# Kernel tuning notes

Hardware: AMD Instinct MI355X
Metric: run time of the kernel (lower is better)

## Reference

```python
import jax, jax.numpy as jnp
import numpy as np

TEMPERATURE = 1.0  # module default current_temperature
TOP_K = 2
NUM_EXPERTS = 64
EPS = 1e-10


def setup_inputs() -> dict:
    key = jax.random.key(0)
    k1, k2 = jax.random.split(key)
    x = jax.random.normal(k1, (4, 4096, 2048), dtype=jnp.float32)
    # nn.Linear(d_model, num_experts) weight has shape [num_experts, d_model]
    W_gate = jax.random.normal(k2, (NUM_EXPERTS, 2048), dtype=jnp.float32) * (1.0 / np.sqrt(2048))
    return {"x": x, "W_gate": W_gate}


def reference(x, W_gate):
    # Gate GEMM: [B,S,D] x [E,D] -> [B,S,E]
    logits = jnp.einsum("bsd,ed->bse", x, W_gate)
    scaled = logits / TEMPERATURE
    # Full distribution over experts (for load-balancing loss)
    router_probs = jax.nn.softmax(scaled, axis=-1)
    # Top-k selection over the expert dim, then renormalize via softmax
    top_k_logits, top_k_indices = jax.lax.top_k(scaled, TOP_K)  # [B,S,K]
    top_k_weights = jax.nn.softmax(top_k_logits, axis=-1)
    # Routing stats (no-grad in torch; plain values here)
    entropy = -jnp.sum(router_probs * jnp.log(router_probs + EPS), axis=-1)
    routing_entropy = entropy.mean()
    selection_confidence = top_k_weights[:, :, 0].mean()
    counts = jnp.zeros((NUM_EXPERTS,), dtype=x.dtype).at[top_k_indices.reshape(-1)].add(1.0)
    expert_utilization = counts / (counts.sum() + EPS)
    return (top_k_weights, top_k_indices, router_probs,
            routing_entropy, selection_confidence, expert_utilization)
```

## Files before the change

kernel.cpp:

```cpp
#include <hip/hip_runtime.h>
#include <math.h>

#define NTOK 16384
#define DIM 2048
#define NEXP 64
#define TB 32
#define NSG 32

#define OFF_W    0
#define OFF_I    32768
#define OFF_P    65536
#define OFF_ENT  1114112
#define OFF_CONF 1114113
#define OFF_UTIL 1114114

typedef short s16x8 __attribute__((ext_vector_type(8)));
typedef float f32x4 __attribute__((ext_vector_type(4)));

__device__ __forceinline__ unsigned short f2bf(float v) {
    unsigned u = __builtin_bit_cast(unsigned, v);
    u = u + 0x7FFFu + ((u >> 16) & 1u);
    return (unsigned short)(u >> 16);
}
__device__ __forceinline__ float bf2f(unsigned short b) {
    return __builtin_bit_cast(float, (unsigned)b << 16);
}

__global__ void router_wsplit(const float* __restrict__ Wg, uint4* __restrict__ wsp,
                              float* __restrict__ out) {
    const int c = blockIdx.x;
    const int t = threadIdx.x;
    if (c == 0 && t < 66) out[OFF_ENT + t] = 0.0f;
    const int nt = t >> 6, l = t & 63;
    const int e  = 16 * nt + (l & 15);
    const int k0 = 32 * c + 8 * (l >> 4);
    const float* src = Wg + (size_t)e * DIM + k0;
    float4 a = *(const float4*)src;
    float4 b = *(const float4*)(src + 4);
    float v[8] = {a.x, a.y, a.z, a.w, b.x, b.y, b.z, b.w};
    unsigned short H[8], M[8], L[8];
    #pragma unroll
    for (int j = 0; j < 8; ++j) {
        H[j] = f2bf(v[j]);  float r = v[j] - bf2f(H[j]);
        M[j] = f2bf(r);     r = r - bf2f(M[j]);
        L[j] = f2bf(r);
    }
    uint4 ph, pm, pl;
    ph.x = H[0] | ((unsigned)H[1] << 16); ph.y = H[2] | ((unsigned)H[3] << 16);
    ph.z = H[4] | ((unsigned)H[5] << 16); ph.w = H[6] | ((unsigned)H[7] << 16);
    pm.x = M[0] | ((unsigned)M[1] << 16); pm.y = M[2] | ((unsigned)M[3] << 16);
    pm.z = M[4] | ((unsigned)M[5] << 16); pm.w = M[6] | ((unsigned)M[7] << 16);
    pl.x = L[0] | ((unsigned)L[1] << 16); pl.y = L[2] | ((unsigned)L[3] << 16);
    pl.z = L[4] | ((unsigned)L[5] << 16); pl.w = L[6] | ((unsigned)L[7] << 16);
    const int idx = c * 256 + t;
    wsp[idx]         = ph;
    wsp[16384 + idx] = pm;
    wsp[32768 + idx] = pl;
}

#define LOADW(W_, c_) { const int b_ = (c_)*256 + np*128 + l;  \
    W_[0] = wq[b_];          W_[1] = wq[b_ + 64];              \
    W_[2] = wq[16384 + b_];  W_[3] = wq[16384 + b_ + 64];      \
    W_[4] = wq[32768 + b_];  W_[5] = wq[32768 + b_ + 64]; }

#define SPLIT8(a0_, a1_, ph_, pm_, pl_) {                                \
    float xv[8] = {a0_.x, a0_.y, a0_.z, a0_.w,                           \
                   a1_.x, a1_.y, a1_.z, a1_.w};                          \
    unsigned hw_[8], mw_[8], lw_[8];                                     \
    _Pragma("unroll")                                                    \
    for (int j = 0; j < 8; ++j) {                                        \
        unsigned u_  = __builtin_bit_cast(unsigned, xv[j]);              \
        unsigned hb_ = u_ & 0xFFFF0000u;                                 \
        float    r_  = xv[j] - __builtin_bit_cast(float, hb_);           \
        unsigned mb_ = __builtin_bit_cast(unsigned, r_) & 0xFFFF0000u;   \
        float    r2_ = r_ - __builtin_bit_cast(float, mb_);              \
        unsigned lb_ = __builtin_bit_cast(unsigned, r2_);                \
        hw_[j] = hb_ >> 16; mw_[j] = mb_ >> 16; lw_[j] = lb_ >> 16;      \
    }                                                                    \
    ph_.x = hw_[0] | (hw_[1] << 16); ph_.y = hw_[2] | (hw_[3] << 16);    \
    ph_.z = hw_[4] | (hw_[5] << 16); ph_.w = hw_[6] | (hw_[7] << 16);    \
    pm_.x = mw_[0] | (mw_[1] << 16); pm_.y = mw_[2] | (mw_[3] << 16);    \
    pm_.z = mw_[4] | (mw_[5] << 16); pm_.w = mw_[6] | (mw_[7] << 16);    \
    pl_.x = lw_[0] | (lw_[1] << 16); pl_.y = lw_[2] | (lw_[3] << 16);    \
    pl_.z = lw_[4] | (lw_[5] << 16); pl_.w = lw_[6] | (lw_[7] << 16);    \
}

#define STAGEW(buf_) {                                                   \
    uint4 ph_, pm_, pl_;                                                 \
    SPLIT8(xr0, xr1, ph_, pm_, pl_);                                     \
    Xp[g][buf_][0][cc][st][sq] = ph_;                                    \
    Xp[g][buf_][1][cc][st][sq] = pm_;                                    \
    Xp[g][buf_][2][cc][st][sq] = pl_;                                    \
}

#define READA(buf_, cc_) {                                               \
    ah = __builtin_bit_cast(s16x8, Xp[g][buf_][0][cc_][tl][sl]);         \
    am = __builtin_bit_cast(s16x8, Xp[g][buf_][1][cc_][tl][sl]);         \
    al = __builtin_bit_cast(s16x8, Xp[g][buf_][2][cc_][tl][sl]);         \
}

#define COMPUTE(W_) {                                                    \
    s16x8 b0h_ = __builtin_bit_cast(s16x8, W_[0]);                       \
    s16x8 b1h_ = __builtin_bit_cast(s16x8, W_[1]);                       \
    s16x8 b0m_ = __builtin_bit_cast(s16x8, W_[2]);                       \
    s16x8 b1m_ = __builtin_bit_cast(s16x8, W_[3]);                       \
    s16x8 b0l_ = __builtin_bit_cast(s16x8, W_[4]);                       \
    s16x8 b1l_ = __builtin_bit_cast(s16x8, W_[5]);                       \
    acc0 = __builtin_amdgcn_mfma_f32_16x16x32_bf16(ah, b0h_, acc0, 0, 0, 0); \
    acc1 = __builtin_amdgcn_mfma_f32_16x16x32_bf16(ah, b1h_, acc1, 0, 0, 0); \
    acc0 = __builtin_amdgcn_mfma_f32_16x16x32_bf16(am, b0h_, acc0, 0, 0, 0); \
    acc1 = __builtin_amdgcn_mfma_f32_16x16x32_bf16(am, b1h_, acc1, 0, 0, 0); \
    acc0 = __builtin_amdgcn_mfma_f32_16x16x32_bf16(ah, b0m_, acc0, 0, 0, 0); \
    acc1 = __builtin_amdgcn_mfma_f32_16x16x32_bf16(ah, b1m_, acc1, 0, 0, 0); \
    acc0 = __builtin_amdgcn_mfma_f32_16x16x32_bf16(am, b0m_, acc0, 0, 0, 0); \
    acc1 = __builtin_amdgcn_mfma_f32_16x16x32_bf16(am, b1m_, acc1, 0, 0, 0); \
    acc0 = __builtin_amdgcn_mfma_f32_16x16x32_bf16(ah, b0l_, acc0, 0, 0, 0); \
    acc1 = __builtin_amdgcn_mfma_f32_16x16x32_bf16(ah, b1l_, acc1, 0, 0, 0); \
    acc0 = __builtin_amdgcn_mfma_f32_16x16x32_bf16(al, b0h_, acc0, 0, 0, 0); \
    acc1 = __builtin_amdgcn_mfma_f32_16x16x32_bf16(al, b1h_, acc1, 0, 0, 0); \
    }

__global__ __launch_bounds__(512, 4) void router_main(
    const float* __restrict__ x, const uint4* __restrict__ wq,
    float* __restrict__ out)
{
    __shared__ __align__(16) uint4 Xp[2][2][3][2][TB][4];
    __shared__ float lg[TB][NEXP + 1];
    __shared__ float m1s[TB], rss[TB];
    __shared__ float s_ent, s_conf, s_cnt[NEXP];

    const int tid = threadIdx.x;
    const int l   = tid & 63;
    const int w   = tid >> 6;
    const int g   = tid >> 8;
    const int lw  = w & 3;
    const int np  = __builtin_amdgcn_readfirstlane(lw >> 1);
    const int tt  = lw & 1;
    const int qd  = l >> 4;
    const int tl  = tt * 16 + (l & 15);
    const int sl  = qd ^ ((tl >> 2) & 3);
    const int t0  = blockIdx.x * TB;
    const int cb  = g * NSG;

    if (tid == 0) { s_ent = 0.0f; s_conf = 0.0f; }
    if (tid < NEXP) s_cnt[tid] = 0.0f;

    const int gtid = tid & 255;
    const int cc  = gtid >> 7;
    const int rr  = gtid & 127;
    const int st  = rr >> 2;
    const int sq  = rr & 3;
    const int gq  = sq ^ ((st >> 2) & 3);
    const float* xsrc = x + (size_t)(t0 + st) * DIM + 32 * cb + 8 * gq;

    f32x4 acc0 = (f32x4)(0.0f), acc1 = (f32x4)(0.0f);
    s16x8 ah, am, al;
    uint4 wA[6], wB[6];
    float4 xr0, xr1;

    xr0 = *(const float4*)(xsrc + cc * 32);
    xr1 = *(const float4*)(xsrc + cc * 32 + 4);
    LOADW(wA, cb + 0); LOADW(wB, cb + 1);
    STAGEW(0);
    xr0 = *(const float4*)(xsrc + (2 + cc) * 32);
    xr1 = *(const float4*)(xsrc + (2 + cc) * 32 + 4);
    __syncthreads();

    for (int s = 0; s < NSG; s += 2) {
        const int buf = (s >> 1) & 1;
        if (s + 2 < NSG) STAGEW(buf ^ 1);
        if (s + 4 < NSG) {
            xr0 = *(const float4*)(xsrc + (s + 4 + cc) * 32);
            xr1 = *(const float4*)(xsrc + (s + 4 + cc) * 32 + 4);
        }
        READA(buf, 0);
        COMPUTE(wA);
        if (s + 2 < NSG) LOADW(wA, cb + s + 2);
        READA(buf, 1);
        COMPUTE(wB);
        if (s + 3 < NSG) LOADW(wB, cb + s + 3);
        asm volatile("s_waitcnt lgkmcnt(0)" ::: "memory");
        __builtin_amdgcn_sched_barrier(0);
        __builtin_amdgcn_s_barrier();
        __builtin_amdgcn_sched_barrier(0);
    }

    if (g == 1) {
        #pragma unroll
        for (int r = 0; r < 4; ++r) {
            lg[tt * 16 + 4 * qd + r][np * 32 + (l & 15)]      = acc0[r];
            lg[tt * 16 + 4 * qd + r][np * 32 + 16 + (l & 15)] = acc1[r];
        }
    }
    __syncthreads();
    if (g == 0) {
        #pragma unroll
        for (int r = 0; r < 4; ++r) {
            lg[tt * 16 + 4 * qd + r][np * 32 + (l & 15)]      += acc0[r];
            lg[tt * 16 + 4 * qd + r][np * 32 + 16 + (l & 15)] += acc1[r];
        }
    }
    __syncthreads();

    if (tid < TB) {
        const int t = tid;
        float m1 = -INFINITY, m2 = -INFINITY;
        int i1 = 0, i2 = 0;
        for (int e = 0; e < NEXP; ++e) {
            float lv = lg[t][e];
            if (lv > m1)      { m2 = m1; i2 = i1; m1 = lv; i1 = e; }
            else if (lv > m2) { m2 = lv; i2 = e; }
        }
        float ssum = 0.0f, tsum = 0.0f;
        for (int e = 0; e < NEXP; ++e) {
            float d = lg[t][e] - m1;
            float ex = __expf(d);
            ssum += ex;
            tsum += d * ex;
        }
        float rs = 1.0f / ssum;
        float H  = logf(ssum) - tsum * rs;
        float e2 = __expf(m2 - m1);
        float rn = 1.0f / (1.0f + e2);
        float w0 = rn, w1v = e2 * rn;
        m1s[t] = m1; rss[t] = rs;

        *(float2*)&out[OFF_W + 2 * (t0 + t)] = make_float2(w0, w1v);
        *(float2*)&out[OFF_I + 2 * (t0 + t)] = make_float2((float)i1, (float)i2);

        atomicAdd(&s_ent,  H);
        atomicAdd(&s_conf, w0);
        atomicAdd(&s_cnt[i1], 1.0f);
        atomicAdd(&s_cnt[i2], 1.0f);
    }
    __syncthreads();

    {
        int t  = tid >> 4;
        int qq = tid & 15;
        float m  = m1s[t];
        float rs = rss[t];
        float4 pr;
        pr.x = __expf(lg[t][4 * qq + 0] - m) * rs;
        pr.y = __expf(lg[t][4 * qq + 1] - m) * rs;
        pr.z = __expf(lg[t][4 * qq + 2] - m) * rs;
        pr.w = __expf(lg[t][4 * qq + 3] - m) * rs;
        *(float4*)&out[OFF_P + (size_t)(t0 + t) * NEXP + 4 * qq] = pr;
    }

    if (tid == 0) {
        atomicAdd(&out[OFF_ENT],  s_ent  * (1.0f / 16384.0f));
        atomicAdd(&out[OFF_CONF], s_conf * (1.0f / 16384.0f));
    }
    if (tid < NEXP)
        atomicAdd(&out[OFF_UTIL + tid], s_cnt[tid] * (1.0f / 32768.0f));
}

extern "C" void kernel_launch(void* const* d_in, const int* in_sizes, int n_in,
                              void* d_out, int out_size, void* d_ws, size_t ws_size,
                              hipStream_t stream) {
    const float* x  = (const float*)d_in[0];
    const float* Wg = (const float*)d_in[1];
    float* out = (float*)d_out;
    (void)in_sizes; (void)n_in; (void)out_size; (void)ws_size;

    router_wsplit<<<dim3(64), dim3(256), 0, stream>>>(Wg, (uint4*)d_ws, out);
    router_main<<<dim3(NTOK / TB), dim3(512), 0, stream>>>(x, (const uint4*)d_ws, out);
}
```

Measured before the change: 231.2 us.

## Load x directly into MFMA registers and split K across four wave groups

```diff
diff --git a/kernel.cpp b/kernel.cpp
--- a/kernel.cpp
+++ b/kernel.cpp
@@ -5,7 +5,8 @@
 #define DIM 2048
 #define NEXP 64
 #define TB 32
-#define NSG 32
+#define KG 4
+#define CPG 16
 
 #define OFF_W    0
 #define OFF_I    32768
@@ -28,10 +29,12 @@
 
 __global__ void router_wsplit(const float* __restrict__ Wg, uint4* __restrict__ wsp,
                               float* __restrict__ out) {
-    const int c = blockIdx.x;
-    const int t = threadIdx.x;
-    if (c == 0 && t < 66) out[OFF_ENT + t] = 0.0f;
-    const int nt = t >> 6, l = t & 63;
+    const int bid = blockIdx.x;
+    const int tid = threadIdx.x;
+    const int c   = bid >> 2;
+    const int gt  = (bid & 3) * 64 + tid;
+    if (c == 0 && gt < 66) out[OFF_ENT + gt] = 0.0f;
+    const int nt = gt >> 6, l = gt & 63;
     const int e  = 16 * nt + (l & 15);
     const int k0 = 32 * c + 8 * (l >> 4);
     const float* src = Wg + (size_t)e * DIM + k0;
@@ -52,21 +55,30 @@
     pm.z = M[4] | ((unsigned)M[5] << 16); pm.w = M[6] | ((unsigned)M[7] << 16);
     pl.x = L[0] | ((unsigned)L[1] << 16); pl.y = L[2] | ((unsigned)L[3] << 16);
     pl.z = L[4] | ((unsigned)L[5] << 16); pl.w = L[6] | ((unsigned)L[7] << 16);
-    const int idx = c * 256 + t;
+    const int idx = c * 256 + gt;
     wsp[idx]         = ph;
     wsp[16384 + idx] = pm;
     wsp[32768 + idx] = pl;
 }
 
-#define LOADW(W_, c_) { const int b_ = (c_)*256 + np*128 + l;  \
-    W_[0] = wq[b_];          W_[1] = wq[b_ + 64];              \
-    W_[2] = wq[16384 + b_];  W_[3] = wq[16384 + b_ + 64];      \
-    W_[4] = wq[32768 + b_];  W_[5] = wq[32768 + b_ + 64]; }
-
-#define SPLIT8(a0_, a1_, ph_, pm_, pl_) {                                \
-    float xv[8] = {a0_.x, a0_.y, a0_.z, a0_.w,                           \
-                   a1_.x, a1_.y, a1_.z, a1_.w};                          \
-    unsigned hw_[8], mw_[8], lw_[8];                                     \
+#define LOADW6(W_, i_) {                         \
+    W_[0] = wb[(i_) * 256];                      \
+    W_[1] = wb[(i_) * 256 + 64];                 \
+    W_[2] = wb[(i_) * 256 + 16384];              \
+    W_[3] = wb[(i_) * 256 + 16384 + 64];         \
+    W_[4] = wb[(i_) * 256 + 32768];              \
+    W_[5] = wb[(i_) * 256 + 32768 + 64]; }
+
+#define LOADX4(X_, i_) {                                   \
+    X_[0] = *(const float4*)(xb0 + (i_) * 32);             \
+    X_[1] = *(const float4*)(xb0 + (i_) * 32 + 4);         \
+    X_[2] = *(const float4*)(xb1 + (i_) * 32);             \
+    X_[3] = *(const float4*)(xb1 + (i_) * 32 + 4); }
+
+#define CONVA(a0_, a1_) {                                                \
+    float xv[8];                                                         \
+    xv[0]=a0_.x; xv[1]=a0_.y; xv[2]=a0_.z; xv[3]=a0_.w;                  \
+    xv[4]=a1_.x; xv[5]=a1_.y; xv[6]=a1_.z; xv[7]=a1_.w;                  \
     _Pragma("unroll")                                                    \
     for (int j = 0; j < 8; ++j) {                                        \
         unsigned u_  = __builtin_bit_cast(unsigned, xv[j]);              \
@@ -75,56 +87,36 @@
         unsigned mb_ = __builtin_bit_cast(unsigned, r_) & 0xFFFF0000u;   \
         float    r2_ = r_ - __builtin_bit_cast(float, mb_);              \
         unsigned lb_ = __builtin_bit_cast(unsigned, r2_);                \
-        hw_[j] = hb_ >> 16; mw_[j] = mb_ >> 16; lw_[j] = lb_ >> 16;      \
-    }                                                                    \
-    ph_.x = hw_[0] | (hw_[1] << 16); ph_.y = hw_[2] | (hw_[3] << 16);    \
-    ph_.z = hw_[4] | (hw_[5] << 16); ph_.w = hw_[6] | (hw_[7] << 16);    \
-    pm_.x = mw_[0] | (mw_[1] << 16); pm_.y = mw_[2] | (mw_[3] << 16);    \
-    pm_.z = mw_[4] | (mw_[5] << 16); pm_.w = mw_[6] | (mw_[7] << 16);    \
-    pl_.x = lw_[0] | (lw_[1] << 16); pl_.y = lw_[2] | (lw_[3] << 16);    \
-    pl_.z = lw_[4] | (lw_[5] << 16); pl_.w = lw_[6] | (lw_[7] << 16);    \
-}
-
-#define STAGEW(buf_) {                                                   \
-    uint4 ph_, pm_, pl_;                                                 \
-    SPLIT8(xr0, xr1, ph_, pm_, pl_);                                     \
-    Xp[g][buf_][0][cc][st][sq] = ph_;                                    \
-    Xp[g][buf_][1][cc][st][sq] = pm_;                                    \
-    Xp[g][buf_][2][cc][st][sq] = pl_;                                    \
-}
-
-#define READA(buf_, cc_) {                                               \
-    ah = __builtin_bit_cast(s16x8, Xp[g][buf_][0][cc_][tl][sl]);         \
-    am = __builtin_bit_cast(s16x8, Xp[g][buf_][1][cc_][tl][sl]);         \
-    al = __builtin_bit_cast(s16x8, Xp[g][buf_][2][cc_][tl][sl]);         \
-}
-
-#define COMPUTE(W_) {                                                    \
+        ah[j] = (short)(hb_ >> 16);                                      \
+        am[j] = (short)(mb_ >> 16);                                      \
+        al[j] = (short)(lb_ >> 16);                                      \
+    } }
+
+#define COMPUTE12(W_, aE_, aO_) {                                        \
     s16x8 b0h_ = __builtin_bit_cast(s16x8, W_[0]);                       \
     s16x8 b1h_ = __builtin_bit_cast(s16x8, W_[1]);                       \
     s16x8 b0m_ = __builtin_bit_cast(s16x8, W_[2]);                       \
     s16x8 b1m_ = __builtin_bit_cast(s16x8, W_[3]);                       \
     s16x8 b0l_ = __builtin_bit_cast(s16x8, W_[4]);                       \
     s16x8 b1l_ = __builtin_bit_cast(s16x8, W_[5]);                       \
-    acc0 = __builtin_amdgcn_mfma_f32_16x16x32_bf16(ah, b0h_, acc0, 0, 0, 0); \
-    acc1 = __builtin_amdgcn_mfma_f32_16x16x32_bf16(ah, b1h_, acc1, 0, 0, 0); \
-    acc0 = __builtin_amdgcn_mfma_f32_16x16x32_bf16(am, b0h_, acc0, 0, 0, 0); \
-    acc1 = __builtin_amdgcn_mfma_f32_16x16x32_bf16(am, b1h_, acc1, 0, 0, 0); \
-    acc0 = __builtin_amdgcn_mfma_f32_16x16x32_bf16(ah, b0m_, acc0, 0, 0, 0); \
-    acc1 = __builtin_amdgcn_mfma_f32_16x16x32_bf16(ah, b1m_, acc1, 0, 0, 0); \
-    acc0 = __builtin_amdgcn_mfma_f32_16x16x32_bf16(am, b0m_, acc0, 0, 0, 0); \
-    acc1 = __builtin_amdgcn_mfma_f32_16x16x32_bf16(am, b1m_, acc1, 0, 0, 0); \
-    acc0 = __builtin_amdgcn_mfma_f32_16x16x32_bf16(ah, b0l_, acc0, 0, 0, 0); \
-    acc1 = __builtin_amdgcn_mfma_f32_16x16x32_bf16(ah, b1l_, acc1, 0, 0, 0); \
-    acc0 = __builtin_amdgcn_mfma_f32_16x16x32_bf16(al, b0h_, acc0, 0, 0, 0); \
-    acc1 = __builtin_amdgcn_mfma_f32_16x16x32_bf16(al, b1h_, acc1, 0, 0, 0); \
+    aE_ = __builtin_amdgcn_mfma_f32_16x16x32_bf16(ah, b0h_, aE_, 0, 0, 0); \
+    aO_ = __builtin_amdgcn_mfma_f32_16x16x32_bf16(ah, b1h_, aO_, 0, 0, 0); \
+    aE_ = __builtin_amdgcn_mfma_f32_16x16x32_bf16(am, b0h_, aE_, 0, 0, 0); \
+    aO_ = __builtin_amdgcn_mfma_f32_16x16x32_bf16(am, b1h_, aO_, 0, 0, 0); \
+    aE_ = __builtin_amdgcn_mfma_f32_16x16x32_bf16(ah, b0m_, aE_, 0, 0, 0); \
+    aO_ = __builtin_amdgcn_mfma_f32_16x16x32_bf16(ah, b1m_, aO_, 0, 0, 0); \
+    aE_ = __builtin_amdgcn_mfma_f32_16x16x32_bf16(am, b0m_, aE_, 0, 0, 0); \
+    aO_ = __builtin_amdgcn_mfma_f32_16x16x32_bf16(am, b1m_, aO_, 0, 0, 0); \
+    aE_ = __builtin_amdgcn_mfma_f32_16x16x32_bf16(ah, b0l_, aE_, 0, 0, 0); \
+    aO_ = __builtin_amdgcn_mfma_f32_16x16x32_bf16(ah, b1l_, aO_, 0, 0, 0); \
+    aE_ = __builtin_amdgcn_mfma_f32_16x16x32_bf16(al, b0h_, aE_, 0, 0, 0); \
+    aO_ = __builtin_amdgcn_mfma_f32_16x16x32_bf16(al, b1h_, aO_, 0, 0, 0); \
     }
 
 __global__ __launch_bounds__(512, 4) void router_main(
     const float* __restrict__ x, const uint4* __restrict__ wq,
     float* __restrict__ out)
 {
-    __shared__ __align__(16) uint4 Xp[2][2][3][2][TB][4];
     __shared__ float lg[TB][NEXP + 1];
     __shared__ float m1s[TB], rss[TB];
     __shared__ float s_ent, s_conf, s_cnt[NEXP];
@@ -132,75 +124,54 @@
     const int tid = threadIdx.x;
     const int l   = tid & 63;
     const int w   = tid >> 6;
-    const int g   = tid >> 8;
-    const int lw  = w & 3;
-    const int np  = __builtin_amdgcn_readfirstlane(lw >> 1);
-    const int tt  = lw & 1;
+    const int g   = __builtin_amdgcn_readfirstlane(w >> 1);
+    const int np  = __builtin_amdgcn_readfirstlane(w & 1);
     const int qd  = l >> 4;
-    const int tl  = tt * 16 + (l & 15);
-    const int sl  = qd ^ ((tl >> 2) & 3);
+    const int tr  = l & 15;
     const int t0  = blockIdx.x * TB;
-    const int cb  = g * NSG;
 
     if (tid == 0) { s_ent = 0.0f; s_conf = 0.0f; }
     if (tid < NEXP) s_cnt[tid] = 0.0f;
 
-    const int gtid = tid & 255;
-    const int cc  = gtid >> 7;
-    const int rr  = gtid & 127;
-    const int st  = rr >> 2;
-    const int sq  = rr & 3;
-    const int gq  = sq ^ ((st >> 2) & 3);
-    const float* xsrc = x + (size_t)(t0 + st) * DIM + 32 * cb + 8 * gq;
-
-    f32x4 acc0 = (f32x4)(0.0f), acc1 = (f32x4)(0.0f);
+    const float* xb0 = x + (size_t)(t0 + tr) * DIM + g * (CPG * 32) + 8 * qd;
+    const float* xb1 = xb0 + 16 * DIM;
+    const uint4* wb  = wq + (size_t)(g * CPG) * 256 + np * 128 + l;
+
+    f32x4 a00 = (f32x4)(0.0f), a01 = (f32x4)(0.0f);
+    f32x4 a10 = (f32x4)(0.0f), a11 = (f32x4)(0.0f);
     s16x8 ah, am, al;
     uint4 wA[6], wB[6];
-    float4 xr0, xr1;
-
-    xr0 = *(const float4*)(xsrc + cc * 32);
-    xr1 = *(const float4*)(xsrc + cc * 32 + 4);
-    LOADW(wA, cb + 0); LOADW(wB, cb + 1);
-    STAGEW(0);
-    xr0 = *(const float4*)(xsrc + (2 + cc) * 32);
-    xr1 = *(const float4*)(xsrc + (2 + cc) * 32 + 4);
-    __syncthreads();
-
-    for (int s = 0; s < NSG; s += 2) {
-        const int buf = (s >> 1) & 1;
-        if (s + 2 < NSG) STAGEW(buf ^ 1);
-        if (s + 4 < NSG) {
-            xr0 = *(const float4*)(xsrc + (s + 4 + cc) * 32);
-            xr1 = *(const float4*)(xsrc + (s + 4 + cc) * 32 + 4);
-        }
-        READA(buf, 0);
-        COMPUTE(wA);
-        if (s + 2 < NSG) LOADW(wA, cb + s + 2);
-        READA(buf, 1);
-        COMPUTE(wB);
-        if (s + 3 < NSG) LOADW(wB, cb + s + 3);
-        asm volatile("s_waitcnt lgkmcnt(0)" ::: "memory");
-        __builtin_amdgcn_sched_barrier(0);
-        __builtin_amdgcn_s_barrier();
-        __builtin_amdgcn_sched_barrier(0);
-    }
-
-    if (g == 1) {
-        #pragma unroll
-        for (int r = 0; r < 4; ++r) {
-            lg[tt * 16 + 4 * qd + r][np * 32 + (l & 15)]      = acc0[r];
-            lg[tt * 16 + 4 * qd + r][np * 32 + 16 + (l & 15)] = acc1[r];
-        }
-    }
-    __syncthreads();
-    if (g == 0) {
-        #pragma unroll
-        for (int r = 0; r < 4; ++r) {
-            lg[tt * 16 + 4 * qd + r][np * 32 + (l & 15)]      += acc0[r];
-            lg[tt * 16 + 4 * qd + r][np * 32 + 16 + (l & 15)] += acc1[r];
-        }
-    }
-    __syncthreads();
+    float4 xA[4], xB[4];
+
+    LOADW6(wA, 0); LOADX4(xA, 0);
+    LOADW6(wB, 1); LOADX4(xB, 1);
+
+    #pragma unroll
+    for (int i = 0; i < CPG; i += 2) {
+        CONVA(xA[0], xA[1]);  COMPUTE12(wA, a00, a01);
+        CONVA(xA[2], xA[3]);  COMPUTE12(wA, a10, a11);
+        if (i + 2 < CPG) { LOADW6(wA, i + 2); LOADX4(xA, i + 2); }
+        CONVA(xB[0], xB[1]);  COMPUTE12(wB, a00, a01);
+        CONVA(xB[2], xB[3]);  COMPUTE12(wB, a10, a11);
+        if (i + 3 < CPG) { LOADW6(wB, i + 3); LOADX4(xB, i + 3); }
+    }
+
+#define WRROWS(op_) { _Pragma("unroll")                                  \
+    for (int r = 0; r < 4; ++r) {                                        \
+        lg[4 * qd + r][np * 32 + tr]           op_ a00[r];               \
+        lg[4 * qd + r][np * 32 + 16 + tr]      op_ a01[r];               \
+        lg[16 + 4 * qd + r][np * 32 + tr]      op_ a10[r];               \
+        lg[16 + 4 * qd + r][np * 32 + 16 + tr] op_ a11[r];               \
+    } }
+    if (g == 3) WRROWS(=);
+    __syncthreads();
+    if (g == 2) WRROWS(+=);
+    __syncthreads();
+    if (g == 1) WRROWS(+=);
+    __syncthreads();
+    if (g == 0) WRROWS(+=);
+    __syncthreads();
+#undef WRROWS
 
     if (tid < TB) {
         const int t = tid;
@@ -264,6 +235,6 @@
     float* out = (float*)d_out;
     (void)in_sizes; (void)n_in; (void)out_size; (void)ws_size;
 
-    router_wsplit<<<dim3(64), dim3(256), 0, stream>>>(Wg, (uint4*)d_ws, out);
+    router_wsplit<<<dim3(256), dim3(64), 0, stream>>>(Wg, (uint4*)d_ws, out);
     router_main<<<dim3(NTOK / TB), dim3(512), 0, stream>>>(x, (const uint4*)d_ws, out);
 }
```

Result: slower. 238.1 us (+3.0%).
